# Kernel optimization log

Hardware: AMD Instinct MI355X
Metric: run time of the kernel (lower is better)

Reference implementation:

```python
import jax, jax.numpy as jnp
import numpy as np


def setup_inputs() -> dict:
    key = jax.random.key(0)
    ks = jax.random.split(key, 6)
    B, S, H = 1, 512, 2048
    NH, D = 16, 128
    S_CACHE = 8192
    TOPK = 16
    hidden_states = jax.random.normal(ks[0], (B, S, H), dtype=jnp.float32)
    Wqkv = jax.random.normal(ks[1], (3 * H, H), dtype=jnp.float32) * 0.02
    Wout = jax.random.normal(ks[2], (H, H), dtype=jnp.float32) * 0.02
    k_cache = jax.random.normal(ks[3], (B, NH, S_CACHE, D), dtype=jnp.float32)
    v_cache = jax.random.normal(ks[4], (B, NH, S_CACHE, D), dtype=jnp.float32)
    position_bias = jax.random.normal(ks[5], (NH, S, S), dtype=jnp.float32) * 0.1
    # causal mask: True = masked out (matches torch masked_fill semantics)
    attention_mask = ~jnp.tril(jnp.ones((S, S), dtype=bool))
    return {
        "hidden_states": hidden_states,
        "Wqkv": Wqkv,
        "Wout": Wout,
        "k_cache": k_cache,
        "v_cache": v_cache,
        "position_bias": position_bias,
        "attention_mask": attention_mask,
        "topk": TOPK,
    }


SIM_THRESHOLD = 0.25  # config.sim_threshold


def reference(hidden_states, Wqkv, Wout, k_cache, v_cache, position_bias,
              attention_mask, topk):
    B, S, H = hidden_states.shape
    NH, D = k_cache.shape[1], k_cache.shape[3]
    scale = 1.0 / jnp.sqrt(jnp.asarray(D, hidden_states.dtype))

    # QKV projection (Linear, no bias): x @ W^T, then split heads
    qkv = jnp.einsum('bsh,oh->bso', hidden_states, Wqkv)
    q, k, v = jnp.split(qkv, 3, axis=-1)
    def to_heads(x):
        return x.reshape(B, S, NH, D).transpose(0, 2, 1, 3)  # [B,NH,S,D]
    q, k, v = to_heads(q), to_heads(k), to_heads(v)

    # local attention scores + alibi-style bias
    scores_local = jnp.einsum('bhqd,bhkd->bhqk', q, k) * scale
    scores_local = scores_local + position_bias[None]  # [B,NH,S,S]

    # cosine-similarity retrieval over long-range cache
    q_n = q / jnp.linalg.norm(q, axis=-1, keepdims=True)
    k_n = k_cache / jnp.linalg.norm(k_cache, axis=-1, keepdims=True)
    sim = jnp.einsum('bhqd,bhkd->bhqk', q_n, k_n)  # [B,NH,S,S_CACHE]
    val, idx = jax.lax.top_k(sim, topk)            # [B,NH,S,topk]
    reshaped_idx = idx.reshape(B, NH, S * topk)

    # gather retrieved K/V
    sel_k = jnp.take_along_axis(k_cache, reshaped_idx[..., None], axis=2)  # [B,NH,S*topk,D]
    sel_v = jnp.take_along_axis(v_cache, reshaped_idx[..., None], axis=2)

    scores_cache = jnp.einsum('bhqd,bhkd->bhqk', q, sel_k) * scale  # [B,NH,S,S*topk]
    neg = jnp.finfo(scores_cache.dtype).min

    # similarity-threshold mask (mask_by_sim=True)
    sim_mask = ~(val > SIM_THRESHOLD)                       # [B,NH,S,topk]
    sim_mask = sim_mask.reshape(B, NH, 1, S * topk)         # broadcast over queries
    scores_cache = jnp.where(sim_mask, neg, scores_cache)

    # block-diagonal external-memory mask: query i attends only to its own topk slots
    rows = jnp.arange(S)[:, None]
    cols_block = jnp.arange(S * topk)[None, :] // topk
    ext_mask = cols_block != rows                           # [S, S*topk], True = masked

    full_mask = jnp.concatenate([ext_mask, attention_mask], axis=1)  # [S, S*topk+S]
    scores = jnp.concatenate([scores_cache, scores_local], axis=-1)
    scores = jnp.where(full_mask[None, None], neg, scores)

    attn = jax.nn.softmax(scores.astype(jnp.float32), axis=-1).astype(v.dtype)
    values = jnp.concatenate([sel_v, v], axis=2)            # [B,NH,S*topk+S,D]
    ctx = jnp.einsum('bhqk,bhkd->bhqd', attn, values)
    ctx = ctx.transpose(0, 2, 1, 3).reshape(B, S, H)
    attn_output = jnp.einsum('bsh,oh->bso', ctx, Wout)
    return attn_output
```

## Files before the change

kernel.cpp:

```cpp
#include <hip/hip_runtime.h>

typedef _Float16 half8 __attribute__((ext_vector_type(8)));
typedef _Float16 half4 __attribute__((ext_vector_type(4)));
typedef _Float16 half2t __attribute__((ext_vector_type(2)));
typedef float f32x4 __attribute__((ext_vector_type(4)));
typedef float f32x2 __attribute__((ext_vector_type(2)));

#define NHEAD 16
#define SEQ 512
#define DIM 128
#define HID 2048
#define SCACHE 8192
#define CAP 64
#define SCALE 0.08838834764831845f
#define NEG_INF (-__builtin_inff())
#define RECMAX 2048

__global__ __launch_bounds__(256) void gemm_xwT(const float* __restrict__ A,
                                                const float* __restrict__ B,
                                                float* __restrict__ Cpart,
                                                int K, int gridN, int kslices) {
  __shared__ __align__(16) _Float16 As[128][84];
  __shared__ __align__(16) _Float16 Bs[128][84];
  int b = blockIdx.x;
  int kblk = b % kslices;
  int nm = b / kslices;
  int nblk = nm % gridN, mblk = nm / gridN;
  int N = gridN * 128;
  int kchunk = K / kslices;
  int t = threadIdx.x;
  int lane = t & 63, wid = t >> 6;
  int wm = (wid >> 1) * 64, wn = (wid & 1) * 64;
  f32x4 acc[4][4] = {};
  const float* Ab = A + (size_t)mblk * 128 * K;
  const float* Bb = B + (size_t)nblk * 128 * K;
  int rowS = t >> 4, c4 = (t & 15) * 4;

  for (int k0 = kblk * kchunk; k0 < kblk * kchunk + kchunk; k0 += 64) {
#pragma unroll
    for (int i = 0; i < 8; ++i) {
      int row = rowS + 16 * i;
      float4 av = *(const float4*)(Ab + (size_t)row * K + k0 + c4);
      float4 bv = *(const float4*)(Bb + (size_t)row * K + k0 + c4);
      half4 ah = {(_Float16)av.x, (_Float16)av.y, (_Float16)av.z, (_Float16)av.w};
      half4 bh = {(_Float16)bv.x, (_Float16)bv.y, (_Float16)bv.z, (_Float16)bv.w};
      *(half4*)&As[row][c4] = ah;
      *(half4*)&Bs[row][c4] = bh;
    }
    __syncthreads();
#pragma unroll
    for (int ks = 0; ks < 2; ++ks) {
      int ko = ks * 32 + (lane >> 4) * 8;
      int rr = lane & 15;
      half8 af[4], bf[4];
#pragma unroll
      for (int i = 0; i < 4; ++i) af[i] = *(const half8*)&As[wm + i * 16 + rr][ko];
#pragma unroll
      for (int j = 0; j < 4; ++j) bf[j] = *(const half8*)&Bs[wn + j * 16 + rr][ko];
#pragma unroll
      for (int i = 0; i < 4; ++i)
#pragma unroll
        for (int j = 0; j < 4; ++j)
          acc[i][j] = __builtin_amdgcn_mfma_f32_16x16x32_f16(af[i], bf[j], acc[i][j], 0, 0, 0);
    }
    __syncthreads();
  }
  float* Cp = Cpart + (size_t)kblk * ((size_t)gridN * 128) * 512;
  int cR = (lane >> 4) * 4, cC = lane & 15;
#pragma unroll
  for (int i = 0; i < 4; ++i)
#pragma unroll
    for (int j = 0; j < 4; ++j) {
      int row = mblk * 128 + wm + i * 16 + cR;
      int col = nblk * 128 + wn + j * 16 + cC;
#pragma unroll
      for (int r = 0; r < 4; ++r)
        Cp[(size_t)(row + r) * N + col] = acc[i][j][r];
    }
}

__global__ __launch_bounds__(256) void reduce_k(const float* __restrict__ part,
                                                float* __restrict__ dst,
                                                int kslices, int ncol, int dstride) {
  size_t e = ((size_t)blockIdx.x * 256 + threadIdx.x) * 4;
  size_t slice = (size_t)512 * ncol;
  f32x4 s = *(const f32x4*)(part + e);
  for (int p = 1; p < kslices; ++p)
    s += *(const f32x4*)(part + (size_t)p * slice + e);
  size_t row = e / ncol;
  int col = (int)(e % ncol);
  *(f32x4*)(dst + row * dstride + col) = s;
}

__global__ __launch_bounds__(256) void split_hilo(const float* __restrict__ src,
                                                  _Float16* __restrict__ hi,
                                                  _Float16* __restrict__ lo) {
  size_t e = ((size_t)blockIdx.x * 256 + threadIdx.x) * 4;
  f32x4 v = *(const f32x4*)(src + e);
  half4 h = {(_Float16)v[0], (_Float16)v[1], (_Float16)v[2], (_Float16)v[3]};
  half4 l = {(_Float16)(v[0] - (float)h[0]), (_Float16)(v[1] - (float)h[1]),
             (_Float16)(v[2] - (float)h[2]), (_Float16)(v[3] - (float)h[3])};
  *(half4*)(hi + e) = h;
  *(half4*)(lo + e) = l;
}

__global__ __launch_bounds__(256) void gemm_q_hi(const _Float16* __restrict__ Ahg,
                                                 const _Float16* __restrict__ Alg,
                                                 const _Float16* __restrict__ Bhg,
                                                 const _Float16* __restrict__ Blg,
                                                 float* __restrict__ C) {
  __shared__ __align__(16) _Float16 Ahs[32][72], Als[32][72];
  __shared__ __align__(16) _Float16 Bhs[32][72], Bls[32][72];
  int b = blockIdx.x;
  int nblk = b & 63, mblk = b >> 6;
  int t = threadIdx.x, lane = t & 63, w = t >> 6;
  int wm = (w >> 1) * 16, wn = (w & 1) * 16;
  int quad = lane >> 4, rr = lane & 15;
  f32x4 acc = {};
  const _Float16* Ab0 = Ahg + (size_t)(mblk * 32) * 2048;
  const _Float16* Ab1 = Alg + (size_t)(mblk * 32) * 2048;
  const _Float16* Bb0 = Bhg + (size_t)(nblk * 32) * 2048;
  const _Float16* Bb1 = Blg + (size_t)(nblk * 32) * 2048;
  int srow = t >> 3, sc = (t & 7) * 8;

  for (int k0 = 0; k0 < 2048; k0 += 64) {
    size_t goff = (size_t)srow * 2048 + k0 + sc;
    *(uint4*)&Ahs[srow][sc] = *(const uint4*)(Ab0 + goff);
    *(uint4*)&Als[srow][sc] = *(const uint4*)(Ab1 + goff);
    *(uint4*)&Bhs[srow][sc] = *(const uint4*)(Bb0 + goff);
    *(uint4*)&Bls[srow][sc] = *(const uint4*)(Bb1 + goff);
    __syncthreads();
#pragma unroll
    for (int ks = 0; ks < 2; ++ks) {
      int ko = ks * 32 + quad * 8;
      half8 afh = *(const half8*)&Ahs[wm + rr][ko];
      half8 afl = *(const half8*)&Als[wm + rr][ko];
      half8 bfh = *(const half8*)&Bhs[wn + rr][ko];
      half8 bfl = *(const half8*)&Bls[wn + rr][ko];
      acc = __builtin_amdgcn_mfma_f32_16x16x32_f16(afl, bfh, acc, 0, 0, 0);
      acc = __builtin_amdgcn_mfma_f32_16x16x32_f16(afh, bfl, acc, 0, 0, 0);
      acc = __builtin_amdgcn_mfma_f32_16x16x32_f16(afh, bfh, acc, 0, 0, 0);
    }
    __syncthreads();
  }
  int row = mblk * 32 + wm + quad * 4;
  int col = nblk * 32 + wn + rr;
#pragma unroll
  for (int r = 0; r < 4; ++r)
    C[(size_t)(row + r) * (3 * HID) + col] = acc[r];
}

__global__ __launch_bounds__(256) void cache_norm(const float* __restrict__ kc,
                                                  _Float16* __restrict__ kn16,
                                                  double* __restrict__ kninv) {
  int w = threadIdx.x >> 6, lane = threadIdx.x & 63;
  int row = blockIdx.x * 4 + w;
  f32x2 v = *(const f32x2*)(kc + (size_t)row * DIM + lane * 2);
  double s = (double)v[0] * v[0] + (double)v[1] * v[1];
#pragma unroll
  for (int off = 32; off; off >>= 1) s += __shfl_xor(s, off);
  float inv = rsqrtf((float)s);
  half2t o = {(_Float16)(v[0] * inv), (_Float16)(v[1] * inv)};
  *(half2t*)(kn16 + (size_t)row * DIM + lane * 2) = o;
  if (lane == 0) kninv[row] = 1.0 / sqrt(s);
}

__global__ __launch_bounds__(256) void prep_local(const float* __restrict__ qkv,
                                                  _Float16* __restrict__ q16,
                                                  _Float16* __restrict__ k16,
                                                  _Float16* __restrict__ qn16) {
  int w = threadIdx.x >> 6, lane = threadIdx.x & 63;
  int rid = blockIdx.x * 4 + w;
  int h = rid >> 9, s = rid & 511;
  const float* qp = qkv + (size_t)s * (3 * HID) + h * DIM + lane * 2;
  f32x2 q = *(const f32x2*)qp;
  f32x2 k = *(const f32x2*)(qp + HID);
  float ss = q[0] * q[0] + q[1] * q[1];
#pragma unroll
  for (int off = 32; off; off >>= 1) ss += __shfl_xor(ss, off);
  float inv = rsqrtf(ss);
  half2t qh = {(_Float16)q[0], (_Float16)q[1]};
  half2t kh = {(_Float16)k[0], (_Float16)k[1]};
  half2t qnh = {(_Float16)(q[0] * inv), (_Float16)(q[1] * inv)};
  *(half2t*)(q16 + (size_t)rid * DIM + lane * 2) = qh;
  *(half2t*)(k16 + (size_t)rid * DIM + lane * 2) = kh;
  *(half2t*)(qn16 + (size_t)rid * DIM + lane * 2) = qnh;
}

__global__ __launch_bounds__(256) void sim_cand(const _Float16* __restrict__ qn16,
                                                const _Float16* __restrict__ kn16,
                                                int* __restrict__ rec,
                                                int* __restrict__ reccnt) {
  __shared__ int ls_buf[RECMAX];
  __shared__ int ls_cnt;
  int b = blockIdx.x;
  int h = b >> 6, cblk = b & 63;
  int t = threadIdx.x, lane = t & 63, w = t >> 6;
  int quad = lane >> 4, rr = lane & 15;
  if (t == 0) ls_cnt = 0;
  __syncthreads();

  half8 bf[2][4];
  {
    const _Float16* kb = kn16 + ((size_t)(h * SCACHE + cblk * 128 + w * 32)) * DIM;
#pragma unroll
    for (int jn = 0; jn < 2; ++jn)
#pragma unroll
      for (int ks = 0; ks < 4; ++ks)
        bf[jn][ks] = *(const half8*)(kb + (size_t)(jn * 16 + rr) * DIM + ks * 32 + quad * 8);
  }

  const _Float16* qbase = qn16 + (size_t)h * SEQ * DIM + (size_t)rr * DIM + quad * 8;

  for (int qt = 0; qt < 8; ++qt) {
    const _Float16* qp = qbase + (size_t)(qt * 64) * DIM;
    f32x4 acc[4][2] = {};
#pragma unroll
    for (int ks = 0; ks < 4; ++ks) {
      half8 af[4];
#pragma unroll
      for (int i = 0; i < 4; ++i)
        af[i] = *(const half8*)(qp + (size_t)(i * 16) * DIM + ks * 32);
#pragma unroll
      for (int i = 0; i < 4; ++i)
#pragma unroll
        for (int j = 0; j < 2; ++j)
          acc[i][j] = __builtin_amdgcn_mfma_f32_16x16x32_f16(af[i], bf[j][ks], acc[i][j], 0, 0, 0);
    }
    int qrow_base = qt * 64 + (quad << 2);
    int key_base = cblk * 128 + w * 32 + rr;
#pragma unroll
    for (int i = 0; i < 4; ++i)
#pragma unroll
      for (int j = 0; j < 2; ++j)
#pragma unroll
        for (int r = 0; r < 4; ++r) {
          float v = acc[i][j][r];
          if (v > 0.249f) {
            int q = qrow_base + i * 16 + r;
            int p = atomicAdd(&ls_cnt, 1);
            if (p < RECMAX) ls_buf[p] = (q << 13) | (key_base + j * 16);
          }
        }
  }
  __syncthreads();
  int total = ls_cnt;
  if (total > RECMAX) total = RECMAX;
  int* rp = rec + (size_t)b * RECMAX;
  for (int e = t; e < total; e += 256) rp[e] = ls_buf[e];
  if (t == 0) reccnt[b] = total;
}

__global__ __launch_bounds__(256) void cand_merge(const int* __restrict__ rec,
                                                  const int* __restrict__ reccnt,
                                                  int* __restrict__ cnt,
                                                  int* __restrict__ cidx) {
  __shared__ int lc[512];
  int h = blockIdx.x;
  int t = threadIdx.x, w = t >> 6, lane = t & 63;
  for (int i = t; i < 512; i += 256) lc[i] = 0;
  __syncthreads();
  for (int s8 = 0; s8 < 16; ++s8) {
    int cblk = s8 * 4 + w;
    int bA = h * 64 + cblk;
    int n = reccnt[bA];
    const int* rp = rec + (size_t)bA * RECMAX;
    for (int e = lane; e < n; e += 64) {
      int rv = rp[e];
      int q = rv >> 13, key = rv & 8191;
      int pos = atomicAdd(&lc[q], 1);
      if (pos < CAP) cidx[((size_t)h * 512 + q) * CAP + pos] = key;
    }
  }
  __syncthreads();
  for (int i = t; i < 512; i += 256) cnt[h * 512 + i] = lc[i];
}

__global__ __launch_bounds__(256) void select_topk(const int* __restrict__ cnt,
                                                   const int* __restrict__ cidx,
                                                   const float* __restrict__ qkv,
                                                   const float* __restrict__ kcache,
                                                   const double* __restrict__ kninv,
                                                   int* __restrict__ sel_idx,
                                                   float* __restrict__ sel_score) {
  int w = threadIdx.x >> 6, lane = threadIdx.x & 63;
  int rowid = blockIdx.x * 4 + w;
  int h = rowid >> 9, s = rowid & 511;
  const float* qp = qkv + (size_t)s * (3 * HID) + h * DIM;

  f32x2 qv2 = *(const f32x2*)(qp + lane * 2);
  double qs = (double)qv2[0] * qv2[0] + (double)qv2[1] * qv2[1];
#pragma unroll
  for (int off = 32; off; off >>= 1) qs += __shfl_xor(qs, off);
  double thr = 0.25 * sqrt(qs);

  int n = min(cnt[rowid], CAP);
  int idx = 0x7fffffff;
  double r = -1e300, d = 0.0;
  if (lane < n) {
    idx = cidx[rowid * CAP + lane];
    const float* kp = kcache + ((size_t)(h * SCACHE + idx)) * DIM;
    double d0 = 0.0, d1 = 0.0;
#pragma unroll
    for (int j = 0; j < DIM; j += 8) {
      f32x4 ka = *(const f32x4*)(kp + j);
      f32x4 kb = *(const f32x4*)(kp + j + 4);
      f32x4 qa = *(const f32x4*)(qp + j);
      f32x4 qb = *(const f32x4*)(qp + j + 4);
      d0 = fma((double)qa[0], (double)ka[0], d0);
      d1 = fma((double)qa[1], (double)ka[1], d1);
      d0 = fma((double)qa[2], (double)ka[2], d0);
      d1 = fma((double)qa[3], (double)ka[3], d1);
      d0 = fma((double)qb[0], (double)kb[0], d0);
      d1 = fma((double)qb[1], (double)kb[1], d1);
      d0 = fma((double)qb[2], (double)kb[2], d0);
      d1 = fma((double)qb[3], (double)kb[3], d1);
    }
    d = d0 + d1;
    r = d * kninv[h * SCACHE + idx];
  }

  int rank = 0;
  for (int j = 0; j < n; ++j) {
    double rj = __shfl(r, j);
    int ij = __shfl(idx, j);
    if (rj > r || (rj == r && ij < idx)) ++rank;
  }
  bool sel = (lane < n) && (rank < 16) && (r > thr);
  unsigned long long m = __ballot(sel);
  int nsel = __popcll(m);
  if (sel) {
    int pos = __popcll(m & ((1ull << lane) - 1));
    sel_idx[rowid * 16 + pos] = idx;
    sel_score[rowid * 16 + pos] = (float)(d * (double)SCALE);
  }
  if (lane >= nsel && lane < 16) {
    sel_idx[rowid * 16 + lane] = 0;
    sel_score[rowid * 16 + lane] = NEG_INF;
  }
}

__global__ __launch_bounds__(256) void attn_part(const float* __restrict__ qkv,
                                                 const _Float16* __restrict__ q16,
                                                 const _Float16* __restrict__ k16,
                                                 const float* __restrict__ bias,
                                                 float* __restrict__ part_m,
                                                 float* __restrict__ part_l,
                                                 float* __restrict__ part_o) {
  __shared__ __align__(16) _Float16 Vs[128][136];
  __shared__ __align__(16) _Float16 Ps[16][136];
  __shared__ float mred[16][4], lred[16][4];

  int pb = blockIdx.x;
  int tt = pb % 80, h = pb / 80;
  int qb, cb;
  if (tt < 8)       { qb = tt;                cb = 0; }
  else if (tt < 24) { int u = tt - 8;  qb = 8 + (u >> 1); cb = u & 1; }
  else if (tt < 48) { int u = tt - 24; int q3 = u / 3; qb = 16 + q3; cb = u - q3 * 3; }
  else              { int u = tt - 48; qb = 24 + (u >> 2); cb = u & 3; }
  int q0 = qb * 16, kc0 = cb * 128;

  int t = threadIdx.x, lane = t & 63, w = t >> 6;
  int quad = lane >> 4, col = lane & 15;

  const float* vbase = qkv + 2 * HID + h * DIM;
#pragma unroll
  for (int i = 0; i < 16; ++i) {
    int idx = t + 256 * i;
    int key = idx & 127, dg = idx >> 7;
    f32x4 vv = *(const f32x4*)(vbase + (size_t)(kc0 + key) * (3 * HID) + dg * 4);
#pragma unroll
    for (int e = 0; e < 4; ++e) Vs[dg * 4 + e][key] = (_Float16)vv[e];
  }

  const _Float16* qbp = q16 + ((size_t)(h * SEQ + q0)) * DIM;
  half8 af[4];
#pragma unroll
  for (int ks = 0; ks < 4; ++ks)
    af[ks] = *(const half8*)(qbp + (size_t)col * DIM + ks * 32 + quad * 8);

  f32x4 acc[2] = {};
#pragma unroll
  for (int jn = 0; jn < 2; ++jn) {
    const _Float16* kp = k16 + ((size_t)(h * SEQ + kc0 + w * 32 + jn * 16 + col)) * DIM;
#pragma unroll
    for (int ks = 0; ks < 4; ++ks) {
      half8 bf = *(const half8*)(kp + ks * 32 + quad * 8);
      acc[jn] = __builtin_amdgcn_mfma_f32_16x16x32_f16(af[ks], bf, acc[jn], 0, 0, 0);
    }
  }
  float s[2][4];
#pragma unroll
  for (int jn = 0; jn < 2; ++jn) {
    int keyg = kc0 + w * 32 + jn * 16 + col;
#pragma unroll
    for (int r = 0; r < 4; ++r) {
      int qrow = q0 + quad * 4 + r;
      float sv = NEG_INF;
      if (keyg <= qrow)
        sv = acc[jn][r] * SCALE + bias[((size_t)h * SEQ + qrow) * SEQ + keyg];
      s[jn][r] = sv;
    }
  }

  float mw[4];
#pragma unroll
  for (int r = 0; r < 4; ++r) {
    float m = fmaxf(s[0][r], s[1][r]);
#pragma unroll
    for (int off = 1; off < 16; off <<= 1) m = fmaxf(m, __shfl_xor(m, off));
    mw[r] = m;
  }
  if (col == 0)
#pragma unroll
    for (int r = 0; r < 4; ++r) mred[quad * 4 + r][w] = mw[r];
  __syncthreads();

  float M[4];
#pragma unroll
  for (int r = 0; r < 4; ++r) {
    int row = quad * 4 + r;
    float m = fmaxf(fmaxf(mred[row][0], mred[row][1]),
                    fmaxf(mred[row][2], mred[row][3]));
    M[r] = m;
    float p0 = __expf(s[0][r] - m);
    float p1 = __expf(s[1][r] - m);
    Ps[row][w * 32 + col] = (_Float16)p0;
    Ps[row][w * 32 + 16 + col] = (_Float16)p1;
    float l = p0 + p1;
#pragma unroll
    for (int off = 1; off < 16; off <<= 1) l += __shfl_xor(l, off);
    if (col == 0) lred[row][w] = l;
  }
  if (w == 0 && col == 0)
#pragma unroll
    for (int r = 0; r < 4; ++r) part_m[pb * 16 + quad * 4 + r] = M[r];
  __syncthreads();

  f32x4 o[2] = {};
#pragma unroll
  for (int jn = 0; jn < 2; ++jn) {
#pragma unroll
    for (int ks = 0; ks < 4; ++ks) {
      half8 a = *(const half8*)&Ps[col][ks * 32 + quad * 8];
      half8 bv = *(const half8*)&Vs[w * 32 + jn * 16 + col][ks * 32 + quad * 8];
      o[jn] = __builtin_amdgcn_mfma_f32_16x16x32_f16(a, bv, o[jn], 0, 0, 0);
    }
  }
#pragma unroll
  for (int jn = 0; jn < 2; ++jn)
#pragma unroll
    for (int r = 0; r < 4; ++r)
      part_o[((size_t)pb * 16 + quad * 4 + r) * 128 + w * 32 + jn * 16 + col] = o[jn][r];
  if (t < 16)
    part_l[pb * 16 + t] = lred[t][0] + lred[t][1] + lred[t][2] + lred[t][3];
}

__global__ __launch_bounds__(256) void attn_merge(const float* __restrict__ part_m,
                                                  const float* __restrict__ part_l,
                                                  const float* __restrict__ part_o,
                                                  const int* __restrict__ sel_idx,
                                                  const float* __restrict__ sel_score,
                                                  const float* __restrict__ vcache,
                                                  float* __restrict__ ctx) {
  int w = threadIdx.x >> 6, lane = threadIdx.x & 63;
  int row = blockIdx.x * 4 + w;
  int h = row >> 9, q = row & 511;
  int qb = q >> 4, r = q & 15;
  int base = (qb < 8) ? qb
           : (qb < 16) ? 8 + 2 * (qb - 8)
           : (qb < 24) ? 24 + 3 * (qb - 16)
                       : 48 + 4 * (qb - 24);
  int ncb = (qb >> 3) + 1;
  int pb0 = h * 80 + base;

  float scv[16], mc = NEG_INF;
#pragma unroll
  for (int j = 0; j < 16; ++j) {
    scv[j] = sel_score[row * 16 + j];
    mc = fmaxf(mc, scv[j]);
  }
  float mi[4];
  float M = mc;
  for (int i = 0; i < ncb; ++i) {
    mi[i] = part_m[(pb0 + i) * 16 + r];
    M = fmaxf(M, mi[i]);
  }
  f32x2 O = {0.f, 0.f};
  float L = 0.f;
  for (int i = 0; i < ncb; ++i) {
    float sc = __expf(mi[i] - M);
    f32x2 ov = *(const f32x2*)(part_o + ((size_t)(pb0 + i) * 16 + r) * 128 + lane * 2);
    O += ov * sc;
    L += part_l[(pb0 + i) * 16 + r] * sc;
  }
#pragma unroll
  for (int j = 0; j < 16; ++j) {
    if (scv[j] > NEG_INF) {
      float wv = __expf(scv[j] - M);
      int idx = sel_idx[row * 16 + j];
      f32x2 v = *(const f32x2*)(vcache + ((size_t)(h * SCACHE + idx)) * DIM + lane * 2);
      O += v * wv;
      L += wv;
    }
  }
  f32x2 res = O * (1.f / L);
  *(f32x2*)(ctx + (size_t)q * HID + h * DIM + lane * 2) = res;
}

extern "C" void kernel_launch(void* const* d_in, const int* in_sizes, int n_in,
                              void* d_out, int out_size, void* d_ws, size_t ws_size,
                              hipStream_t stream) {
  const float* hidden = (const float*)d_in[0];
  const float* Wqkv   = (const float*)d_in[1];
  const float* Wout   = (const float*)d_in[2];
  const float* kcache = (const float*)d_in[3];
  const float* vcache = (const float*)d_in[4];
  const float* bias   = (const float*)d_in[5];

  char* ws = (char*)d_ws;
  size_t off = 0;
  float*    qkv   = (float*)(ws + off);    off += (size_t)SEQ * 3 * HID * 4;
  _Float16* q16   = (_Float16*)(ws + off); off += (size_t)NHEAD * SEQ * DIM * 2;
  _Float16* k16   = (_Float16*)(ws + off); off += (size_t)NHEAD * SEQ * DIM * 2;
  _Float16* qn16  = (_Float16*)(ws + off); off += (size_t)NHEAD * SEQ * DIM * 2;
  _Float16* kn16  = (_Float16*)(ws + off); off += (size_t)NHEAD * SCACHE * DIM * 2;
  double*   kninv = (double*)(ws + off);   off += (size_t)NHEAD * SCACHE * 8;
  int*      ccnt  = (int*)(ws + off);      off += (size_t)NHEAD * SEQ * 4;
  int*      cidx  = (int*)(ws + off);      off += (size_t)NHEAD * SEQ * CAP * 4;
  int*      selidx  = (int*)(ws + off);    off += (size_t)NHEAD * SEQ * 16 * 4;
  float*    selsc   = (float*)(ws + off);  off += (size_t)NHEAD * SEQ * 16 * 4;
  float*    ctx   = (float*)(ws + off);    off += (size_t)SEQ * HID * 4;
  float*    pm    = (float*)(ws + off);    off += (size_t)1280 * 16 * 4;
  float*    pl    = (float*)(ws + off);    off += (size_t)1280 * 16 * 4;
  float*    po    = (float*)(ws + off);    off += (size_t)1280 * 16 * 128 * 4;
  int*      rec    = (int*)po;
  int*      reccnt = rec + (size_t)1024 * RECMAX;
  float*    gpart = (float*)(ws + off);
  _Float16* Ahg = (_Float16*)gpart;
  _Float16* Alg = Ahg + (size_t)SEQ * HID;
  _Float16* Bhg = Alg + (size_t)SEQ * HID;
  _Float16* Blg = Bhg + (size_t)HID * HID;

  cache_norm<<<dim3(NHEAD * SCACHE / 4), dim3(256), 0, stream>>>(kcache, kn16, kninv);
  gemm_xwT<<<dim3(4 * 32 * 4), dim3(256), 0, stream>>>(hidden, Wqkv + (size_t)2048 * 2048,
                                                       gpart, 2048, 32, 4);
  reduce_k<<<dim3(SEQ * 4096 / 1024), dim3(256), 0, stream>>>(gpart, qkv + 2048, 4, 4096,
                                                              3 * HID);
  split_hilo<<<dim3(SEQ * HID / 1024), dim3(256), 0, stream>>>(hidden, Ahg, Alg);
  split_hilo<<<dim3(HID * HID / 1024), dim3(256), 0, stream>>>(Wqkv, Bhg, Blg);
  gemm_q_hi<<<dim3(1024), dim3(256), 0, stream>>>(Ahg, Alg, Bhg, Blg, qkv);
  prep_local<<<dim3(NHEAD * SEQ / 4), dim3(256), 0, stream>>>(qkv, q16, k16, qn16);
  sim_cand<<<dim3(NHEAD * 64), dim3(256), 0, stream>>>(qn16, kn16, rec, reccnt);
  cand_merge<<<dim3(NHEAD), dim3(256), 0, stream>>>(rec, reccnt, ccnt, cidx);
  select_topk<<<dim3(NHEAD * SEQ / 4), dim3(256), 0, stream>>>(ccnt, cidx, qkv, kcache,
                                                               kninv, selidx, selsc);
  attn_part<<<dim3(16 * 80), dim3(256), 0, stream>>>(qkv, q16, k16, bias, pm, pl, po);
  attn_merge<<<dim3(NHEAD * SEQ / 4), dim3(256), 0, stream>>>(pm, pl, po, selidx, selsc,
                                                              vcache, ctx);
  gemm_xwT<<<dim3(4 * 16 * 8), dim3(256), 0, stream>>>(ctx, Wout, gpart, 2048, 16, 8);
  reduce_k<<<dim3(SEQ * 2048 / 1024), dim3(256), 0, stream>>>(gpart, (float*)d_out, 8, 2048,
                                                              2048);
}
```

Baseline: 468.6 us.

## Split sim_cand over query quarters with LDS-staged swizzled Q tiles and XCD mapping

The similarity candidate kernel now launches 4096 blocks, each covering 128 queries by 128 cache keys instead of all 512 queries. The Q tile is staged once into XOR-swizzled shared memory rather than re-read from global memory per MFMA step. Block indices are remapped so neighbouring cache blocks land on the same XCD. The per-block record buffer shrinks to 512 entries and the merge kernel is updated to the new indexing, which raises the chance of overflowing and dropping candidates if a block has many hits.

```diff
diff --git a/kernel.cpp b/kernel.cpp
--- a/kernel.cpp
+++ b/kernel.cpp
@@ -14,7 +14,7 @@
 #define CAP 64
 #define SCALE 0.08838834764831845f
 #define NEG_INF (-__builtin_inff())
-#define RECMAX 2048
+#define RECMAX 512
 
 __global__ __launch_bounds__(256) void gemm_xwT(const float* __restrict__ A,
                                                 const float* __restrict__ B,
@@ -191,18 +191,21 @@
                                                 const _Float16* __restrict__ kn16,
                                                 int* __restrict__ rec,
                                                 int* __restrict__ reccnt) {
+  __shared__ __align__(16) _Float16 As[128 * 128];
   __shared__ int ls_buf[RECMAX];
   __shared__ int ls_cnt;
   int b = blockIdx.x;
-  int h = b >> 6, cblk = b & 63;
+  int xcd = b & 7, slot = b >> 3;
+  int mq = slot & 3;
+  int p = (slot >> 2) * 8 + xcd;
+  int h = p >> 6, nblk = p & 63;
   int t = threadIdx.x, lane = t & 63, w = t >> 6;
   int quad = lane >> 4, rr = lane & 15;
   if (t == 0) ls_cnt = 0;
-  __syncthreads();
 
   half8 bf[2][4];
   {
-    const _Float16* kb = kn16 + ((size_t)(h * SCACHE + cblk * 128 + w * 32)) * DIM;
+    const _Float16* kb = kn16 + ((size_t)(h * SCACHE + nblk * 128 + w * 32)) * DIM;
 #pragma unroll
     for (int jn = 0; jn < 2; ++jn)
 #pragma unroll
@@ -210,39 +213,52 @@
         bf[jn][ks] = *(const half8*)(kb + (size_t)(jn * 16 + rr) * DIM + ks * 32 + quad * 8);
   }
 
-  const _Float16* qbase = qn16 + (size_t)h * SEQ * DIM + (size_t)rr * DIM + quad * 8;
-
-  for (int qt = 0; qt < 8; ++qt) {
-    const _Float16* qp = qbase + (size_t)(qt * 64) * DIM;
-    f32x4 acc[4][2] = {};
-#pragma unroll
-    for (int ks = 0; ks < 4; ++ks) {
-      half8 af[4];
-#pragma unroll
-      for (int i = 0; i < 4; ++i)
-        af[i] = *(const half8*)(qp + (size_t)(i * 16) * DIM + ks * 32);
-#pragma unroll
-      for (int i = 0; i < 4; ++i)
-#pragma unroll
-        for (int j = 0; j < 2; ++j)
-          acc[i][j] = __builtin_amdgcn_mfma_f32_16x16x32_f16(af[i], bf[j][ks], acc[i][j], 0, 0, 0);
-    }
-    int qrow_base = qt * 64 + (quad << 2);
-    int key_base = cblk * 128 + w * 32 + rr;
-#pragma unroll
-    for (int i = 0; i < 4; ++i)
-#pragma unroll
-      for (int j = 0; j < 2; ++j)
-#pragma unroll
-        for (int r = 0; r < 4; ++r) {
-          float v = acc[i][j][r];
-          if (v > 0.249f) {
-            int q = qrow_base + i * 16 + r;
-            int p = atomicAdd(&ls_cnt, 1);
-            if (p < RECMAX) ls_buf[p] = (q << 13) | (key_base + j * 16);
-          }
+  {
+    const _Float16* qA = qn16 + ((size_t)(h * SEQ + mq * 128)) * DIM;
+    uint4 sreg[8];
+#pragma unroll
+    for (int i = 0; i < 8; ++i) {
+      int f = t + 256 * i;
+      sreg[i] = *(const uint4*)(qA + (size_t)(f >> 4) * DIM + (f & 15) * 8);
+    }
+#pragma unroll
+    for (int i = 0; i < 8; ++i) {
+      int f = t + 256 * i;
+      int row = f >> 4, c = f & 15;
+      *(uint4*)&As[row * DIM + ((c ^ (row & 7)) * 8)] = sreg[i];
+    }
+  }
+  __syncthreads();
+
+  f32x4 acc[8][2] = {};
+#pragma unroll
+  for (int i = 0; i < 8; ++i) {
+    int R = i * 16 + rr;
+    half8 af[4];
+#pragma unroll
+    for (int ks = 0; ks < 4; ++ks)
+      af[ks] = *(const half8*)&As[R * DIM + (((ks * 4 + quad) ^ (rr & 7)) * 8)];
+#pragma unroll
+    for (int jn = 0; jn < 2; ++jn)
+#pragma unroll
+      for (int ks = 0; ks < 4; ++ks)
+        acc[i][jn] = __builtin_amdgcn_mfma_f32_16x16x32_f16(af[ks], bf[jn][ks], acc[i][jn], 0, 0, 0);
+  }
+
+#pragma unroll
+  for (int i = 0; i < 8; ++i)
+#pragma unroll
+    for (int jn = 0; jn < 2; ++jn)
+#pragma unroll
+      for (int r = 0; r < 4; ++r) {
+        float v = acc[i][jn][r];
+        if (v > 0.249f) {
+          int q = mq * 128 + i * 16 + quad * 4 + r;
+          int key = nblk * 128 + w * 32 + jn * 16 + rr;
+          int pq = atomicAdd(&ls_cnt, 1);
+          if (pq < RECMAX) ls_buf[pq] = (q << 13) | key;
         }
-  }
+      }
   __syncthreads();
   int total = ls_cnt;
   if (total > RECMAX) total = RECMAX;
@@ -260,9 +276,10 @@
   int t = threadIdx.x, w = t >> 6, lane = t & 63;
   for (int i = t; i < 512; i += 256) lc[i] = 0;
   __syncthreads();
-  for (int s8 = 0; s8 < 16; ++s8) {
-    int cblk = s8 * 4 + w;
-    int bA = h * 64 + cblk;
+  for (int u = w; u < 256; u += 4) {
+    int s = u >> 2, mq = u & 3;
+    int p = h * 64 + s;
+    int bA = (p & 7) + 8 * (((p >> 3) << 2) + mq);
     int n = reccnt[bA];
     const int* rp = rec + (size_t)bA * RECMAX;
     for (int e = lane; e < n; e += 64) {
@@ -535,7 +552,7 @@
   float*    pl    = (float*)(ws + off);    off += (size_t)1280 * 16 * 4;
   float*    po    = (float*)(ws + off);    off += (size_t)1280 * 16 * 128 * 4;
   int*      rec    = (int*)po;
-  int*      reccnt = rec + (size_t)1024 * RECMAX;
+  int*      reccnt = rec + (size_t)4096 * RECMAX;
   float*    gpart = (float*)(ws + off);
   _Float16* Ahg = (_Float16*)gpart;
   _Float16* Alg = Ahg + (size_t)SEQ * HID;
@@ -551,7 +568,7 @@
   split_hilo<<<dim3(HID * HID / 1024), dim3(256), 0, stream>>>(Wqkv, Bhg, Blg);
   gemm_q_hi<<<dim3(1024), dim3(256), 0, stream>>>(Ahg, Alg, Bhg, Blg, qkv);
   prep_local<<<dim3(NHEAD * SEQ / 4), dim3(256), 0, stream>>>(qkv, q16, k16, qn16);
-  sim_cand<<<dim3(NHEAD * 64), dim3(256), 0, stream>>>(qn16, kn16, rec, reccnt);
+  sim_cand<<<dim3(4096), dim3(256), 0, stream>>>(qn16, kn16, rec, reccnt);
   cand_merge<<<dim3(NHEAD), dim3(256), 0, stream>>>(rec, reccnt, ccnt, cidx);
   select_topk<<<dim3(NHEAD * SEQ / 4), dim3(256), 0, stream>>>(ccnt, cidx, qkv, kcache,
                                                                kninv, selidx, selsc);
```

After: 463.9 us. No clear change (-1.0%).
